# Performance work log

Measured on AMD Instinct MI355X. Metric: run time of the kernel, lower is better.

## Reference

```python
import jax, jax.numpy as jnp
import numpy as np

N = 50000      # nodes
E = 1_000_000  # edges (avg degree 20)
D = 64         # hidden dim
L = 3          # num dynamics layers
LN_EPS = 1e-5


def layernorm(h, g, b):
    mu = jnp.mean(h, axis=-1, keepdims=True)
    var = jnp.mean(jnp.square(h - mu), axis=-1, keepdims=True)
    return (h - mu) * jax.lax.rsqrt(var + LN_EPS) * g + b


def transformer_conv(h, src, dst, Wq, bq, Wk, bk, Wv, bv, Ws, bs):
    # PyG TransformerConv, heads=1, concat=False, beta=False, root_weight=True
    n = h.shape[0]
    d = Wq.shape[1]
    q = h @ Wq + bq            # [N, D] queries (dst side)
    k = h @ Wk + bk            # [N, D] keys   (src side)
    v = h @ Wv + bv            # [N, D] values (src side)
    logits = jnp.sum(q[dst] * k[src], axis=-1) / jnp.sqrt(jnp.asarray(d, h.dtype))  # [E]
    # segment softmax over incoming edges of each dst node
    m = jax.ops.segment_max(logits, dst, num_segments=n)      # [N]
    e = jnp.exp(logits - m[dst])                               # [E]
    s = jax.ops.segment_sum(e, dst, num_segments=n)            # [N]
    a = e / s[dst]                                             # [E]
    agg = jax.ops.segment_sum(a[:, None] * v[src], dst, num_segments=n)  # [N, D]
    return agg + h @ Ws + bs   # root/skip connection


def setup_inputs() -> dict:
    key = jax.random.key(0)
    ks = jax.random.split(key, 24)
    w = lambda k, shape: (jax.random.normal(k, shape, jnp.float32) * 0.05)
    inp = {
        "x": jax.random.normal(ks[0], (N, D), jnp.float32),
        "edge_index": jax.random.randint(ks[1], (2, E), 0, N, jnp.int32),
        # input_proj conv params
        "Wq0": w(ks[2], (D, D)), "bq0": w(ks[3], (D,)),
        "Wk0": w(ks[4], (D, D)), "bk0": w(ks[5], (D,)),
        "Wv0": w(ks[6], (D, D)), "bv0": w(ks[7], (D,)),
        "Ws0": w(ks[8], (D, D)), "bs0": w(ks[9], (D,)),
        "ln0_g": jnp.ones((D,), jnp.float32), "ln0_b": jnp.zeros((D,), jnp.float32),
        # stacked dynamics conv params [L, ...]
        "Wq": w(ks[10], (L, D, D)), "bq": w(ks[11], (L, D)),
        "Wk": w(ks[12], (L, D, D)), "bk": w(ks[13], (L, D)),
        "Wv": w(ks[14], (L, D, D)), "bv": w(ks[15], (L, D)),
        "Ws": w(ks[16], (L, D, D)), "bs": w(ks[17], (L, D)),
        "ln_g": jnp.ones((L, D), jnp.float32), "ln_b": jnp.zeros((L, D), jnp.float32),
    }
    return inp


def reference(x, edge_index, Wq0, bq0, Wk0, bk0, Wv0, bv0, Ws0, bs0, ln0_g, ln0_b,
              Wq, bq, Wk, bk, Wv, bv, Ws, bs, ln_g, ln_b):
    src, dst = edge_index[0], edge_index[1]
    h = transformer_conv(x, src, dst, Wq0, bq0, Wk0, bk0, Wv0, bv0, Ws0, bs0)
    h = jax.nn.relu(layernorm(h, ln0_g, ln0_b))
    # dropout is identity in eval mode
    for i in range(L):
        hi = transformer_conv(h, src, dst, Wq[i], bq[i], Wk[i], bk[i],
                              Wv[i], bv[i], Ws[i], bs[i])
        h = jax.nn.relu(layernorm(hi + h, ln_g[i], ln_b[i]))
    return h
```

## Files before the change

### kernel.cpp

```cpp
#include <hip/hip_runtime.h>
#include <math.h>

#define NN 50000
#define NE 1000000
#define CAP 64
#define LN_EPS 1e-5f
#define ROW_TILES 3125
#define GEMM_BLOCKS 782
#define BE_T 250112
#define ELL_BLOCKS 977

typedef __attribute__((ext_vector_type(8))) short short8;
typedef __attribute__((ext_vector_type(8))) unsigned short ushort8;
typedef __attribute__((ext_vector_type(4))) float f32x4;

__device__ __forceinline__ unsigned short f2bf(float f) {
  union { float f; unsigned u; } v; v.f = f;
  unsigned r = v.u + 0x7FFF + ((v.u >> 16) & 1);
  return (unsigned short)(r >> 16);
}
__device__ __forceinline__ float bf2f(unsigned short b) {
  union { unsigned u; float f; } v; v.u = ((unsigned)b) << 16;
  return v.f;
}

__global__ __launch_bounds__(256) void wprep(
    const float* __restrict__ Wq0, const float* __restrict__ bq0,
    const float* __restrict__ Wk0, const float* __restrict__ bk0,
    const float* __restrict__ Wv0, const float* __restrict__ bv0,
    const float* __restrict__ Ws0, const float* __restrict__ bs0,
    const float* __restrict__ WqL, const float* __restrict__ bqL,
    const float* __restrict__ WkL, const float* __restrict__ bkL,
    const float* __restrict__ WvL, const float* __restrict__ bvL,
    const float* __restrict__ WsL, const float* __restrict__ bsL,
    unsigned short* __restrict__ Wt, float* __restrict__ Bc) {
  int tid = blockIdx.x * 256 + threadIdx.x;
  if (tid >= 4 * 256 * 64) return;
  int lyr = tid >> 14;
  int rem = tid & 16383;
  int c = rem >> 6;
  int k = rem & 63;
  int m = c >> 6;
  int n = c & 63;
  const float *W, *B;
  if (lyr == 0) {
    const float* Wm[4] = {Wq0, Wk0, Wv0, Ws0};
    const float* Bm[4] = {bq0, bk0, bv0, bs0};
    W = Wm[m]; B = Bm[m];
  } else {
    const float* Wm[4] = {WqL, WkL, WvL, WsL};
    const float* Bm[4] = {bqL, bkL, bvL, bsL};
    W = Wm[m] + (size_t)(lyr - 1) * 4096;
    B = Bm[m] + (size_t)(lyr - 1) * 64;
  }
  Wt[(size_t)lyr * 16384 + (size_t)c * 64 + k] = f2bf(W[(size_t)k * 64 + n]);
  if (k == 0) Bc[lyr * 256 + c] = B[n];
}

__global__ __launch_bounds__(256) void gemm_qkvs(
    const float* __restrict__ h, const unsigned short* __restrict__ Wt,
    const float* __restrict__ Bc, unsigned short* __restrict__ Qb,
    unsigned int* __restrict__ KVb, float* __restrict__ Sf,
    const int* __restrict__ ei, int* __restrict__ cursor,
    unsigned short* __restrict__ ell, int nGemm) {
  __shared__ unsigned short lw[256 * 72];
  int tid = threadIdx.x;

  if ((int)blockIdx.x >= nGemm) {
    int t = (blockIdx.x - nGemm) * 256 + tid;
    int e[4]; bool v[4]; int s[4], d[4], p[4];
#pragma unroll
    for (int i = 0; i < 4; ++i) { e[i] = t + i * BE_T; v[i] = e[i] < NE; }
#pragma unroll
    for (int i = 0; i < 4; ++i) {
      if (v[i]) { s[i] = ei[e[i]]; d[i] = ei[NE + e[i]]; }
    }
#pragma unroll
    for (int i = 0; i < 4; ++i) {
      if (v[i]) p[i] = atomicAdd(&cursor[d[i]], 1);
    }
#pragma unroll
    for (int i = 0; i < 4; ++i) {
      if (v[i] && p[i] < CAP) ell[(size_t)d[i] * CAP + p[i]] = (unsigned short)s[i];
    }
    return;
  }

#pragma unroll
  for (int it = 0; it < 8; ++it) {
    int id = it * 256 + tid;
    int row = id >> 3, cc = id & 7;
    float4 src = *reinterpret_cast<const float4*>(Wt + (size_t)row * 64 + cc * 8);
    *reinterpret_cast<float4*>(lw + (size_t)row * 72 + cc * 8) = src;
  }
  __syncthreads();

  int wave = tid >> 6, lane = tid & 63;
  int tile = blockIdx.x * 4 + wave;
  if (tile >= ROW_TILES) return;
  int lo = lane & 15, hi = lane >> 4;
  int row = tile * 16 + lo;
  const float* hrow = h + (size_t)row * 64;

  auto packA = [&](const float* p) {
    float4 x = *reinterpret_cast<const float4*>(p);
    float4 y = *reinterpret_cast<const float4*>(p + 4);
    short8 r;
    r[0] = (short)f2bf(x.x); r[1] = (short)f2bf(x.y);
    r[2] = (short)f2bf(x.z); r[3] = (short)f2bf(x.w);
    r[4] = (short)f2bf(y.x); r[5] = (short)f2bf(y.y);
    r[6] = (short)f2bf(y.z); r[7] = (short)f2bf(y.w);
    return r;
  };
  short8 a0 = packA(hrow + hi * 8);
  short8 a1 = packA(hrow + 32 + hi * 8);

  int rb = tile * 16 + hi * 4;

  auto mm = [&](int brow, float bias) {
    f32x4 acc = {bias, bias, bias, bias};
    const unsigned short* wr = lw + (size_t)brow * 72 + hi * 8;
    short8 b0 = *reinterpret_cast<const short8*>(wr);
    short8 b1 = *reinterpret_cast<const short8*>(wr + 32);
    acc = __builtin_amdgcn_mfma_f32_16x16x32_bf16(a0, b0, acc, 0, 0, 0);
    acc = __builtin_amdgcn_mfma_f32_16x16x32_bf16(a1, b1, acc, 0, 0, 0);
    return acc;
  };

#pragma unroll
  for (int ct = 0; ct < 4; ++ct) {
    int col = ct * 16 + lo;
    f32x4 acc = mm(col, Bc[col]);
#pragma unroll
    for (int r = 0; r < 4; ++r) Qb[(size_t)(rb + r) * 64 + col] = f2bf(acc[r]);
  }
#pragma unroll
  for (int cg = 0; cg < 4; ++cg) {
    int col = cg * 16 + lo;
    f32x4 aK = mm(64 + col, Bc[64 + col]);
    f32x4 aV = mm(128 + col, Bc[128 + col]);
#pragma unroll
    for (int r = 0; r < 4; ++r) {
      unsigned int pk = (unsigned int)f2bf(aK[r]) | ((unsigned int)f2bf(aV[r]) << 16);
      KVb[(size_t)(rb + r) * 64 + col] = pk;
    }
  }
#pragma unroll
  for (int ct = 0; ct < 4; ++ct) {
    int col = ct * 16 + lo;
    f32x4 acc = mm(192 + col, Bc[192 + col]);
#pragma unroll
    for (int r = 0; r < 4; ++r) Sf[(size_t)(rb + r) * 64 + col] = acc[r];
  }
}

__global__ __launch_bounds__(256) void edge_fused(
    const unsigned short* __restrict__ Qb, const unsigned short* __restrict__ KVb,
    const float* __restrict__ Sf,
    const unsigned short* __restrict__ ell, const int* __restrict__ cursor,
    const float* __restrict__ ln_g, const float* __restrict__ ln_b,
    const float* __restrict__ h_res, float* __restrict__ h_out, int use_res) {
  int node = blockIdx.x * 4 + (threadIdx.x >> 6);
  if (node >= NN) return;
  int lane = threadIdx.x & 63;
  int g = lane >> 4, t = lane & 15;

  int deg = cursor[node];
  if (deg > CAP) deg = CAP;
  const unsigned short* lst = ell + (size_t)node * CAP;

  ushort4 qv = *reinterpret_cast<const ushort4*>(Qb + (size_t)node * 64 + t * 4);
  float q0 = bf2f(qv.x), q1 = bf2f(qv.y), q2 = bf2f(qv.z), q3 = bf2f(qv.w);

  int passes = (deg + 3) >> 2;

  auto ldkv = [&](int p) {
    int slot = p * 4 + g;
    int src = (slot < deg) ? (int)lst[slot] : 0;
    return *reinterpret_cast<const ushort8*>(KVb + (size_t)src * 128 + t * 8);
  };

  float4 acc = {0.f, 0.f, 0.f, 0.f};
  float ssum = 0.f;
  ushort8 b0 = ldkv(0);
  ushort8 b1 = ldkv(1);
  for (int p = 0; p < passes; ++p) {
    ushort8 b2 = ldkv(p + 2);
    bool valid = (p * 4 + g) < deg;
    float dp = q0 * bf2f(b0[0]) + q1 * bf2f(b0[2]) +
               q2 * bf2f(b0[4]) + q3 * bf2f(b0[6]);
    dp += __shfl_xor(dp, 1, 64);
    dp += __shfl_xor(dp, 2, 64);
    dp += __shfl_xor(dp, 4, 64);
    dp += __shfl_xor(dp, 8, 64);
    float w = valid ? __expf(dp * 0.125f) : 0.f;
    ssum += w;
    acc.x = fmaf(w, bf2f(b0[1]), acc.x);
    acc.y = fmaf(w, bf2f(b0[3]), acc.y);
    acc.z = fmaf(w, bf2f(b0[5]), acc.z);
    acc.w = fmaf(w, bf2f(b0[7]), acc.w);
    b0 = b1; b1 = b2;
  }
#pragma unroll
  for (int off = 16; off <= 32; off <<= 1) {
    acc.x += __shfl_xor(acc.x, off, 64);
    acc.y += __shfl_xor(acc.y, off, 64);
    acc.z += __shfl_xor(acc.z, off, 64);
    acc.w += __shfl_xor(acc.w, off, 64);
    ssum  += __shfl_xor(ssum, off, 64);
  }
  float inv = (ssum > 0.f) ? (1.f / ssum) : 0.f;

  float4 s4 = *reinterpret_cast<const float4*>(Sf + (size_t)node * 64 + t * 4);
  float4 o;
  o.x = acc.x * inv + s4.x;
  o.y = acc.y * inv + s4.y;
  o.z = acc.z * inv + s4.z;
  o.w = acc.w * inv + s4.w;
  if (use_res) {
    float4 r4 = *reinterpret_cast<const float4*>(h_res + (size_t)node * 64 + t * 4);
    o.x += r4.x; o.y += r4.y; o.z += r4.z; o.w += r4.w;
  }

  float sum = o.x + o.y + o.z + o.w;
  sum += __shfl_xor(sum, 1, 64);
  sum += __shfl_xor(sum, 2, 64);
  sum += __shfl_xor(sum, 4, 64);
  sum += __shfl_xor(sum, 8, 64);
  float mu = sum * (1.f / 64.f);
  float dx = o.x - mu, dy = o.y - mu, dz = o.z - mu, dw = o.w - mu;
  float vs = dx * dx + dy * dy + dz * dz + dw * dw;
  vs += __shfl_xor(vs, 1, 64);
  vs += __shfl_xor(vs, 2, 64);
  vs += __shfl_xor(vs, 4, 64);
  vs += __shfl_xor(vs, 8, 64);
  float rstd = rsqrtf(vs * (1.f / 64.f) + LN_EPS);
  float4 gg = *reinterpret_cast<const float4*>(ln_g + t * 4);
  float4 bb = *reinterpret_cast<const float4*>(ln_b + t * 4);
  float4 y;
  y.x = fmaxf(dx * rstd * gg.x + bb.x, 0.f);
  y.y = fmaxf(dy * rstd * gg.y + bb.y, 0.f);
  y.z = fmaxf(dz * rstd * gg.z + bb.z, 0.f);
  y.w = fmaxf(dw * rstd * gg.w + bb.w, 0.f);
  *reinterpret_cast<float4*>(h_out + (size_t)node * 64 + t * 4) = y;
}

extern "C" void kernel_launch(void* const* d_in, const int* in_sizes, int n_in,
                              void* d_out, int out_size, void* d_ws, size_t ws_size,
                              hipStream_t stream) {
  const float* x    = (const float*)d_in[0];
  const int*   ei   = (const int*)d_in[1];
  const float* Wq0  = (const float*)d_in[2];
  const float* bq0  = (const float*)d_in[3];
  const float* Wk0  = (const float*)d_in[4];
  const float* bk0  = (const float*)d_in[5];
  const float* Wv0  = (const float*)d_in[6];
  const float* bv0  = (const float*)d_in[7];
  const float* Ws0  = (const float*)d_in[8];
  const float* bs0  = (const float*)d_in[9];
  const float* ln0g = (const float*)d_in[10];
  const float* ln0b = (const float*)d_in[11];
  const float* WqL  = (const float*)d_in[12];
  const float* bqL  = (const float*)d_in[13];
  const float* WkL  = (const float*)d_in[14];
  const float* bkL  = (const float*)d_in[15];
  const float* WvL  = (const float*)d_in[16];
  const float* bvL  = (const float*)d_in[17];
  const float* WsL  = (const float*)d_in[18];
  const float* bsL  = (const float*)d_in[19];
  const float* lnG  = (const float*)d_in[20];
  const float* lnB  = (const float*)d_in[21];

  float* h = (float*)d_out;

  char* ws = (char*)d_ws;
  size_t off = 0;
  unsigned short* Qb = (unsigned short*)(ws + off);  off += (size_t)NN * 64 * 2;
  float* Sf = (float*)(ws + off);                    off += (size_t)NN * 64 * 4;
  unsigned int* KVb = (unsigned int*)(ws + off);     off += (size_t)NN * 128 * 2;
  unsigned short* ell = (unsigned short*)(ws + off); off += (size_t)NN * CAP * 2;
  int* cursor = (int*)(ws + off);                    off += (size_t)NN * 4;
  unsigned short* Wt = (unsigned short*)(ws + off);  off += (size_t)4 * 256 * 64 * 2;
  float* Bc = (float*)(ws + off);                    off += (size_t)4 * 256 * 4;

  hipMemsetAsync(cursor, 0, NN * sizeof(int), stream);
  wprep<<<256, 256, 0, stream>>>(Wq0, bq0, Wk0, bk0, Wv0, bv0, Ws0, bs0,
                                 WqL, bqL, WkL, bkL, WvL, bvL, WsL, bsL, Wt, Bc);

  for (int layer = 0; layer < 4; ++layer) {
    const float* hin = (layer == 0) ? x : h;
    const float* lg = (layer == 0) ? ln0g : lnG + (size_t)(layer - 1) * 64;
    const float* lb = (layer == 0) ? ln0b : lnB + (size_t)(layer - 1) * 64;
    int extra = (layer == 0) ? ELL_BLOCKS : 0;
    gemm_qkvs<<<GEMM_BLOCKS + extra, 256, 0, stream>>>(
        hin, Wt + (size_t)layer * 16384, Bc + (size_t)layer * 256,
        Qb, KVb, Sf, ei, cursor, ell, GEMM_BLOCKS);
    edge_fused<<<(NN + 3) / 4, 256, 0, stream>>>(
        Qb, (const unsigned short*)KVb, Sf, ell, cursor, lg, lb, h, h,
        layer > 0 ? 1 : 0);
  }
}
```

Before: 392.5 us.

## Scatter ELL column-major then transpose; read weights from global; deepen KV prefetch

Edge scatter now writes the ELL adjacency column-major (slot-major across nodes), and a new transpose kernel converts it to row-major before the first edge pass. The goal is to reduce write conflicts from the random atomic scatter. The GEMM drops its LDS weight staging and barrier and reads B fragments directly from global memory/cache. The edge kernel prefetches one more KV pass ahead to hide gather latency. These bring an extra kernel launch and workspace buffer, and the GEMM now depends on cache hits for weights.

```diff
diff --git a/kernel.cpp b/kernel.cpp
--- a/kernel.cpp
+++ b/kernel.cpp
@@ -9,6 +9,7 @@
 #define GEMM_BLOCKS 782
 #define BE_T 250112
 #define ELL_BLOCKS 977
+#define TR_BLOCKS 782
 
 typedef __attribute__((ext_vector_type(8))) short short8;
 typedef __attribute__((ext_vector_type(8))) unsigned short ushort8;
@@ -57,13 +58,35 @@
   if (k == 0) Bc[lyr * 256 + c] = B[n];
 }
 
+__global__ __launch_bounds__(256) void ell_transpose(
+    const unsigned short* __restrict__ ell_c, unsigned short* __restrict__ ell_r) {
+  __shared__ unsigned short t[64 * 66];
+  int n0 = blockIdx.x * 64;
+  int tid = threadIdx.x;
+#pragma unroll
+  for (int it = 0; it < 16; ++it) {
+    int idx = it * 256 + tid;
+    int p = idx >> 6, i = idx & 63;
+    int n = n0 + i;
+    unsigned short v = (n < NN) ? ell_c[(size_t)p * NN + n] : (unsigned short)0;
+    t[i * 66 + p] = v;
+  }
+  __syncthreads();
+#pragma unroll
+  for (int it = 0; it < 16; ++it) {
+    int idx = it * 256 + tid;
+    int i = idx >> 6, p = idx & 63;
+    int n = n0 + i;
+    if (n < NN) ell_r[(size_t)n * 64 + p] = t[i * 66 + p];
+  }
+}
+
 __global__ __launch_bounds__(256) void gemm_qkvs(
     const float* __restrict__ h, const unsigned short* __restrict__ Wt,
     const float* __restrict__ Bc, unsigned short* __restrict__ Qb,
     unsigned int* __restrict__ KVb, float* __restrict__ Sf,
     const int* __restrict__ ei, int* __restrict__ cursor,
-    unsigned short* __restrict__ ell, int nGemm) {
-  __shared__ unsigned short lw[256 * 72];
+    unsigned short* __restrict__ ell_c, int nGemm) {
   int tid = threadIdx.x;
 
   if ((int)blockIdx.x >= nGemm) {
@@ -81,19 +104,11 @@
     }
 #pragma unroll
     for (int i = 0; i < 4; ++i) {
-      if (v[i] && p[i] < CAP) ell[(size_t)d[i] * CAP + p[i]] = (unsigned short)s[i];
+      if (v[i] && p[i] < CAP)
+        ell_c[(size_t)p[i] * NN + d[i]] = (unsigned short)s[i];
     }
     return;
   }
-
-#pragma unroll
-  for (int it = 0; it < 8; ++it) {
-    int id = it * 256 + tid;
-    int row = id >> 3, cc = id & 7;
-    float4 src = *reinterpret_cast<const float4*>(Wt + (size_t)row * 64 + cc * 8);
-    *reinterpret_cast<float4*>(lw + (size_t)row * 72 + cc * 8) = src;
-  }
-  __syncthreads();
 
   int wave = tid >> 6, lane = tid & 63;
   int tile = blockIdx.x * 4 + wave;
@@ -119,7 +134,7 @@
 
   auto mm = [&](int brow, float bias) {
     f32x4 acc = {bias, bias, bias, bias};
-    const unsigned short* wr = lw + (size_t)brow * 72 + hi * 8;
+    const unsigned short* wr = Wt + (size_t)brow * 64 + hi * 8;
     short8 b0 = *reinterpret_cast<const short8*>(wr);
     short8 b1 = *reinterpret_cast<const short8*>(wr + 32);
     acc = __builtin_amdgcn_mfma_f32_16x16x32_bf16(a0, b0, acc, 0, 0, 0);
@@ -184,8 +199,9 @@
   float ssum = 0.f;
   ushort8 b0 = ldkv(0);
   ushort8 b1 = ldkv(1);
+  ushort8 b2 = ldkv(2);
   for (int p = 0; p < passes; ++p) {
-    ushort8 b2 = ldkv(p + 2);
+    ushort8 b3 = ldkv(p + 3);
     bool valid = (p * 4 + g) < deg;
     float dp = q0 * bf2f(b0[0]) + q1 * bf2f(b0[2]) +
                q2 * bf2f(b0[4]) + q3 * bf2f(b0[6]);
@@ -199,7 +215,7 @@
     acc.y = fmaf(w, bf2f(b0[3]), acc.y);
     acc.z = fmaf(w, bf2f(b0[5]), acc.z);
     acc.w = fmaf(w, bf2f(b0[7]), acc.w);
-    b0 = b1; b1 = b2;
+    b0 = b1; b1 = b2; b2 = b3;
   }
 #pragma unroll
   for (int off = 16; off <= 32; off <<= 1) {
@@ -275,13 +291,14 @@
 
   char* ws = (char*)d_ws;
   size_t off = 0;
-  unsigned short* Qb = (unsigned short*)(ws + off);  off += (size_t)NN * 64 * 2;
-  float* Sf = (float*)(ws + off);                    off += (size_t)NN * 64 * 4;
-  unsigned int* KVb = (unsigned int*)(ws + off);     off += (size_t)NN * 128 * 2;
-  unsigned short* ell = (unsigned short*)(ws + off); off += (size_t)NN * CAP * 2;
-  int* cursor = (int*)(ws + off);                    off += (size_t)NN * 4;
-  unsigned short* Wt = (unsigned short*)(ws + off);  off += (size_t)4 * 256 * 64 * 2;
-  float* Bc = (float*)(ws + off);                    off += (size_t)4 * 256 * 4;
+  unsigned short* Qb = (unsigned short*)(ws + off);    off += (size_t)NN * 64 * 2;
+  float* Sf = (float*)(ws + off);                      off += (size_t)NN * 64 * 4;
+  unsigned int* KVb = (unsigned int*)(ws + off);       off += (size_t)NN * 128 * 2;
+  unsigned short* ell_r = (unsigned short*)(ws + off); off += (size_t)NN * CAP * 2;
+  unsigned short* ell_c = (unsigned short*)(ws + off); off += (size_t)CAP * NN * 2;
+  int* cursor = (int*)(ws + off);                      off += (size_t)NN * 4;
+  unsigned short* Wt = (unsigned short*)(ws + off);    off += (size_t)4 * 256 * 64 * 2;
+  float* Bc = (float*)(ws + off);                      off += (size_t)4 * 256 * 4;
 
   hipMemsetAsync(cursor, 0, NN * sizeof(int), stream);
   wprep<<<256, 256, 0, stream>>>(Wq0, bq0, Wk0, bk0, Wv0, bv0, Ws0, bs0,
@@ -294,9 +311,11 @@
     int extra = (layer == 0) ? ELL_BLOCKS : 0;
     gemm_qkvs<<<GEMM_BLOCKS + extra, 256, 0, stream>>>(
         hin, Wt + (size_t)layer * 16384, Bc + (size_t)layer * 256,
-        Qb, KVb, Sf, ei, cursor, ell, GEMM_BLOCKS);
+        Qb, KVb, Sf, ei, cursor, ell_c, GEMM_BLOCKS);
+    if (layer == 0)
+      ell_transpose<<<TR_BLOCKS, 256, 0, stream>>>(ell_c, ell_r);
     edge_fused<<<(NN + 3) / 4, 256, 0, stream>>>(
-        Qb, (const unsigned short*)KVb, Sf, ell, cursor, lg, lb, h, h,
+        Qb, (const unsigned short*)KVb, Sf, ell_r, cursor, lg, lb, h, h,
         layer > 0 ? 1 : 0);
   }
 }
```

Result: slower. 441.9 us (+12.6%).
